# Kernel tuning notes

Measured on AMD Instinct MI355X. Metric: run time of the kernel, lower is better.

## Reference

```python
import jax, jax.numpy as jnp
import numpy as np
import math

N_HEADS = 8
D_EMBED = 512
D_CROSS = 768
D_HEAD = D_EMBED // N_HEADS


def _conv1x1(w, b, t):
    # 1x1 conv == pointwise matmul over channel dim. t: [B, Cin, H, W], w: [Cout, Cin]
    out = jnp.einsum('oc,bchw->bohw', w, t)
    return out + b[None, :, None, None]


def setup_inputs() -> dict:
    key = jax.random.key(0)
    ks = jax.random.split(key, 10)
    s = 0.02
    return {
        'x': jax.random.normal(ks[0], (8, D_EMBED, 32, 32), dtype=jnp.float32),
        'y': jax.random.normal(ks[1], (8, D_CROSS, 32, 32), dtype=jnp.float32),
        'w_q': jax.random.normal(ks[2], (D_EMBED, D_EMBED), dtype=jnp.float32) * s,
        'b_q': jnp.zeros((D_EMBED,), dtype=jnp.float32),
        'w_k': jax.random.normal(ks[3], (D_EMBED, D_CROSS), dtype=jnp.float32) * s,
        'b_k': jnp.zeros((D_EMBED,), dtype=jnp.float32),
        'w_v': jax.random.normal(ks[4], (D_EMBED, D_CROSS), dtype=jnp.float32) * s,
        'b_v': jnp.zeros((D_EMBED,), dtype=jnp.float32),
        'w_o': jax.random.normal(ks[5], (D_EMBED, D_EMBED), dtype=jnp.float32) * s,
        'b_o': jnp.zeros((D_EMBED,), dtype=jnp.float32),
    }


def reference(x, y, w_q, b_q, w_k, b_k, w_v, b_v, w_o, b_o):
    B, C, H, W = x.shape
    N = H * W
    q = _conv1x1(w_q, b_q, x)  # [B, C, H, W]
    k = _conv1x1(w_k, b_k, y)
    v = _conv1x1(w_v, b_v, y)
    # flat reshape [B, C, H, W] -> [B, nH, d_head, N] (row-major, matches torch .view)
    q = q.reshape(B, N_HEADS, D_HEAD, N)
    k = k.reshape(B, N_HEADS, D_HEAD, N)
    v = v.reshape(B, N_HEADS, D_HEAD, N)
    # attn = q^T k / sqrt(d_head): [B, nH, N, N]
    scores = jnp.einsum('bhdq,bhdk->bhqk', q, k) / math.sqrt(D_HEAD)
    attn = jax.nn.softmax(scores, axis=-1)
    # out = attn @ v^T : [B, nH, N, d_head]
    out = jnp.einsum('bhqk,bhdk->bhqd', attn, v)
    # faithful quirk: flat reshape (no transpose back) to [B, C, H, W]
    out = out.reshape(B, N_HEADS * D_HEAD, H, W)
    return _conv1x1(w_o, b_o, out)
```

## Files before the change

### kernel.cpp

```cpp
#include <hip/hip_runtime.h>
#include <cstddef>
#include <cstdint>


typedef short bs8 __attribute__((ext_vector_type(8)));
typedef short bs4 __attribute__((ext_vector_type(4)));
typedef float fx4 __attribute__((ext_vector_type(4)));

#define MFMA16(a, b, c) __builtin_amdgcn_mfma_f32_16x16x32_bf16((a), (b), (c), 0, 0, 0)

#define GLOAD_LDS16(g, l)                                                  \
  __builtin_amdgcn_global_load_lds(                                        \
      (const __attribute__((address_space(1))) void*)(g),                  \
      (__attribute__((address_space(3))) void*)(l), 16, 0, 0)

__device__ __forceinline__ short f2b(float f) {
  unsigned u = __builtin_bit_cast(unsigned, f);
  u = (u + 0x7fff + ((u >> 16) & 1)) >> 16;
  return (short)u;
}

__device__ __forceinline__ unsigned cvt_pk_bf16(float lo, float hi) {
  unsigned r;
  asm("v_cvt_pk_bf16_f32 %0, %1, %2" : "=v"(r) : "v"(lo), "v"(hi));
  return r;
}

__device__ __forceinline__ float exp2_fast(float x) {
  float r;
  asm("v_exp_f32 %0, %1" : "=v"(r) : "v"(x));
  return r;
}

#define QSCALE 0.1803368801111244f

__global__ __launch_bounds__(256) void prep(
    const float* __restrict__ w_q, const float* __restrict__ w_k,
    const float* __restrict__ w_v, const float* __restrict__ w_o,
    short* __restrict__ wdst,
    const float* __restrict__ x, short* __restrict__ xt,
    const float* __restrict__ y, short* __restrict__ yt)
{
  __shared__ short T[64][72];
  const int bid = blockIdx.x;
  const int t = threadIdx.x;

  if (bid < 1280) {
    const int i = bid * 1024 + t * 4;
    const float* src; int off;
    if (i < 262144)       { src = w_q; off = 0; }
    else if (i < 655360)  { src = w_k; off = 262144; }
    else if (i < 1048576) { src = w_v; off = 655360; }
    else                  { src = w_o; off = 1048576; }
    float4 f = *(const float4*)(src + (i - off));
    bs4 o; o[0] = f2b(f.x); o[1] = f2b(f.y); o[2] = f2b(f.z); o[3] = f2b(f.w);
    *(bs4*)(wdst + i) = o;
    return;
  }

  const float* src; short* dst; int C, nt, ct, b;
  if (bid < 2304) {
    const int local = bid - 1280;
    src = x; dst = xt; C = 512;
    nt = local & 15; ct = (local >> 4) & 7; b = local >> 7;
  } else {
    const int local = bid - 2304;
    src = y; dst = yt; C = 768;
    nt = local & 15; const int rest = local >> 4; ct = rest % 12; b = rest / 12;
  }

  const size_t srcBase = ((size_t)b * C + ct * 64) * 1024 + nt * 64;
  #pragma unroll
  for (int p = 0; p < 4; ++p) {
    const int lin = p * 256 + t;
    const int row = lin >> 4;
    const int seg = lin & 15;
    float4 f = *(const float4*)(src + srcBase + (size_t)row * 1024 + seg * 4);
    T[seg * 4 + 0][row] = f2b(f.x);
    T[seg * 4 + 1][row] = f2b(f.y);
    T[seg * 4 + 2][row] = f2b(f.z);
    T[seg * 4 + 3][row] = f2b(f.w);
  }
  __syncthreads();
  const size_t dstBase = ((size_t)b * 1024 + nt * 64) * C + ct * 64;
  #pragma unroll
  for (int p = 0; p < 2; ++p) {
    const int lin = p * 256 + t;
    const int row = lin >> 3;
    const int seg = lin & 7;
    *(bs8*)(dst + dstBase + (size_t)row * C + seg * 8) = *(const bs8*)&T[row][seg * 8];
  }
}

__global__ __launch_bounds__(256) void tcast_b(
    const short* __restrict__ src, short* __restrict__ dst, int C)
{
  __shared__ short T[64][72];
  const int t = threadIdx.x;
  const int nt = blockIdx.x, ct = blockIdx.y, b = blockIdx.z;
  const size_t srcBase = ((size_t)b * C + ct * 64) * 1024 + nt * 64;
  #pragma unroll
  for (int p = 0; p < 4; ++p) {
    const int lin = p * 256 + t;
    const int row = lin >> 4;
    const int seg = lin & 15;
    bs4 v = *(const bs4*)(src + srcBase + (size_t)row * 1024 + seg * 4);
    #pragma unroll
    for (int j = 0; j < 4; ++j) T[seg * 4 + j][row] = v[j];
  }
  __syncthreads();
  const size_t dstBase = ((size_t)b * 1024 + nt * 64) * C + ct * 64;
  #pragma unroll
  for (int p = 0; p < 2; ++p) {
    const int lin = p * 256 + t;
    const int row = lin >> 3;
    const int seg = lin & 7;
    *(bs8*)(dst + dstBase + (size_t)row * C + seg * 8) = *(const bs8*)&T[row][seg * 8];
  }
}

template<int MODE, int MTL2>
__device__ __forceinline__ void gemm2_body(
    short* As0, short* As1, short* Bs0, short* Bs1, int hw, int tid,
    const short* __restrict__ W, const short* __restrict__ Xt,
    const float* __restrict__ bias, const float* __restrict__ bias2,
    void* __restrict__ Cout, void* __restrict__ Cout2, int K, float scale)
{
  const int wid = tid >> 6, l = tid & 63;
  const int swz = (hw & 7) * (8 << MTL2) + (hw >> 3);
  const int n0 = (swz & 7) * 128;
  const int m0 = ((swz >> 3) & ((1 << MTL2) - 1)) * 128;
  const int b  = swz >> (3 + MTL2);
  const int wm = wid >> 2, wn = wid & 3;

  const int lrow = l >> 3;
  const int swz8 = ((l & 7) ^ lrow) * 8;
  const int x7 = l & 7;

  const short* Wg = W + (size_t)m0 * K;
  const short* Xg = Xt + ((size_t)b * 1024 + n0) * K;

  fx4 acc[4][2] = {};
  const int NK = K >> 6;

  #pragma unroll
  for (int j = 0; j < 2; ++j) {
    const int rb = j * 64 + wid * 8;
    const int row = rb + lrow;
    GLOAD_LDS16(Wg + (size_t)row * K + swz8, As0 + rb * 64);
    GLOAD_LDS16(Xg + (size_t)row * K + swz8, Bs0 + rb * 64);
  }
  __syncthreads();

  auto gstep = [&](const short* AsC, const short* BsC, short* AsN, short* BsN,
                   int kn, bool pre) {
    if (pre) {
      #pragma unroll
      for (int j = 0; j < 2; ++j) {
        const int rb = j * 64 + wid * 8;
        const int row = rb + lrow;
        GLOAD_LDS16(Wg + (size_t)row * K + kn + swz8, AsN + rb * 64);
        GLOAD_LDS16(Xg + (size_t)row * K + kn + swz8, BsN + rb * 64);
      }
    }
    #pragma unroll
    for (int kb = 0; kb < 2; ++kb) {
      bs8 af[4], bfr[2];
      const int u = (kb * 4 + (l >> 4)) ^ x7;
      #pragma unroll
      for (int ms = 0; ms < 4; ++ms) {
        const int rr = wm * 64 + ms * 16 + (l & 15);
        af[ms] = *(const bs8*)&AsC[rr * 64 + u * 8];
      }
      #pragma unroll
      for (int ns = 0; ns < 2; ++ns) {
        const int rr = wn * 32 + ns * 16 + (l & 15);
        bfr[ns] = *(const bs8*)&BsC[rr * 64 + u * 8];
      }
      #pragma unroll
      for (int ms = 0; ms < 4; ++ms)
        #pragma unroll
        for (int ns = 0; ns < 2; ++ns)
          acc[ms][ns] = MFMA16(af[ms], bfr[ns], acc[ms][ns]);
    }
    __syncthreads();
  };

  const int NK2 = NK >> 1;
  for (int p = 0; p < NK2; ++p) {
    gstep(As0, Bs0, As1, Bs1, (2 * p + 1) * 64, true);
    gstep(As1, Bs1, As0, Bs0, (2 * p + 2) * 64, (2 * p + 2) < NK);
  }

  #pragma unroll
  for (int ms = 0; ms < 4; ++ms) {
    #pragma unroll
    for (int ns = 0; ns < 2; ++ns) {
      const int n = n0 + wn * 32 + ns * 16 + (l & 15);
      const int mb = m0 + wm * 64 + ms * 16 + (l >> 4) * 4;
      if (MODE == 0) {
        const float f0 = (acc[ms][ns][0] + bias[mb + 0]) * scale;
        const float f1 = (acc[ms][ns][1] + bias[mb + 1]) * scale;
        const float f2 = (acc[ms][ns][2] + bias[mb + 2]) * scale;
        const float f3 = (acc[ms][ns][3] + bias[mb + 3]) * scale;
        uint2 od; od.x = cvt_pk_bf16(f0, f1); od.y = cvt_pk_bf16(f2, f3);
        short* dst = (short*)Cout + (((size_t)b * 8 + (mb >> 6)) * 1024 + n) * 64 + (mb & 63);
        *(uint2*)dst = od;
      } else if (MODE == 2) {
        #pragma unroll
        for (int r = 0; r < 4; ++r)
          ((float*)Cout)[((size_t)b * 512 + mb + r) * 1024 + n] = acc[ms][ns][r] + bias[mb + r];
      } else {
        if (mb < 512) {
          const float f0 = acc[ms][ns][0] + bias[mb + 0];
          const float f1 = acc[ms][ns][1] + bias[mb + 1];
          const float f2 = acc[ms][ns][2] + bias[mb + 2];
          const float f3 = acc[ms][ns][3] + bias[mb + 3];
          uint2 od; od.x = cvt_pk_bf16(f0, f1); od.y = cvt_pk_bf16(f2, f3);
          short* dst = (short*)Cout + (((size_t)b * 8 + (mb >> 6)) * 1024 + n) * 64 + (mb & 63);
          *(uint2*)dst = od;
        } else {
          const int c = mb - 512;
          #pragma unroll
          for (int r = 0; r < 4; ++r)
            ((short*)Cout2)[((size_t)b * 512 + c + r) * 1024 + n] = f2b(acc[ms][ns][r] + bias2[c + r]);
        }
      }
    }
  }
}

__global__ __launch_bounds__(512) void gemm_qkv(
    const short* __restrict__ wq, const short* __restrict__ wkv,
    const short* __restrict__ xt, const short* __restrict__ yt,
    const float* __restrict__ b_q, const float* __restrict__ b_k,
    const float* __restrict__ b_v,
    short* __restrict__ Qw, short* __restrict__ Kw, short* __restrict__ Vw)
{
  __shared__ short As[2][128 * 64];
  __shared__ short Bs[2][128 * 64];
  if (blockIdx.x < 256)
    gemm2_body<0, 2>(As[0], As[1], Bs[0], Bs[1], blockIdx.x, threadIdx.x,
                     wq, xt, b_q, nullptr, (void*)Qw, nullptr, 512, QSCALE);
  else
    gemm2_body<3, 3>(As[0], As[1], Bs[0], Bs[1], blockIdx.x - 256, threadIdx.x,
                     wkv, yt, b_k, b_v, (void*)Kw, (void*)Vw, 768, 1.0f);
}

__global__ __launch_bounds__(512) void gemm_o(
    const short* __restrict__ wo, const short* __restrict__ Ot,
    const float* __restrict__ b_o, float* __restrict__ out)
{
  __shared__ short As[2][128 * 64];
  __shared__ short Bs[2][128 * 64];
  gemm2_body<2, 2>(As[0], As[1], Bs[0], Bs[1], blockIdx.x, threadIdx.x,
                   wo, Ot, b_o, nullptr, (void*)out, nullptr, 512, 1.0f);
}

__global__ __launch_bounds__(256) void attn_mfma(
    const short* __restrict__ Q, const short* __restrict__ Kt,
    const short* __restrict__ V, short* __restrict__ O)
{
  __shared__ short Ks[2][64 * 64];
  __shared__ short Vs[2][64 * 64];
  __shared__ short Ps[4][16 * 64];

  const int t = threadIdx.x, wid = t >> 6, l = t & 63;
  const int hw = blockIdx.x;
  const int swzb = (hw & 7) * 128 + (hw >> 3);
  const int qt = swzb & 15, h = (swzb >> 4) & 7, b = swzb >> 7;
  const int q0 = qt * 64 + wid * 16;
  const size_t bh = (size_t)b * 8 + h;

  const short* Qg = Q + (bh * 1024 + q0) * 64;
  const short* Kg = Kt + bh * 1024 * 64;
  const short* Vg = V + bh * 64 * 1024;

  const int g = l >> 4;
  const int q = l & 15;
  const int x7 = q & 7;
  const int lrow = l >> 3;
  const int swz8 = ((l & 7) ^ lrow) * 8;
  short* Pw = Ps[wid];

  bs8 qf[2];
  #pragma unroll
  for (int db = 0; db < 2; ++db)
    qf[db] = *(const bs8*)(Qg + (size_t)q * 64 + db * 32 + g * 8);

  #pragma unroll
  for (int j = 0; j < 2; ++j) {
    const int rbase = wid * 16 + j * 8;
    const int row = rbase + lrow;
    GLOAD_LDS16(Kg + (size_t)row * 64 + swz8, &Ks[0][rbase * 64]);
    GLOAD_LDS16(Vg + (size_t)row * 1024 + swz8, &Vs[0][rbase * 64]);
  }
  __syncthreads();

  float l_part = 0.f;
  fx4 oacc[4] = {};

  auto tile = [&](const short* KsC, const short* VsC, short* KsN, short* VsN,
                  int ktn, bool pre) {
    if (pre) {
      const int k0n = ktn * 64;
      #pragma unroll
      for (int j = 0; j < 2; ++j) {
        const int rbase = wid * 16 + j * 8;
        const int row = rbase + lrow;
        GLOAD_LDS16(Kg + (size_t)(k0n + row) * 64 + swz8, KsN + rbase * 64);
        GLOAD_LDS16(Vg + (size_t)row * 1024 + k0n + swz8, VsN + rbase * 64);
      }
    }

    fx4 s[4] = {};
    __builtin_amdgcn_s_setprio(1);
    #pragma unroll
    for (int ks = 0; ks < 4; ++ks) {
      const int rr = ks * 16 + q;
      #pragma unroll
      for (int db = 0; db < 2; ++db) {
        bs8 kf = *(const bs8*)&KsC[rr * 64 + ((db * 4 + g) ^ x7) * 8];
        s[ks] = MFMA16(kf, qf[db], s[ks]);
      }
    }
    __builtin_amdgcn_s_setprio(0);

    #pragma unroll
    for (int ks = 0; ks < 4; ++ks)
      #pragma unroll
      for (int r = 0; r < 4; ++r) {
        const float e = exp2_fast(s[ks][r]);
        s[ks][r] = e;
        l_part += e;
      }

    #pragma unroll
    for (int ks = 0; ks < 4; ++ks) {
      uint2 pd;
      pd.x = cvt_pk_bf16(s[ks][0], s[ks][1]);
      pd.y = cvt_pk_bf16(s[ks][2], s[ks][3]);
      const int u16 = ks * 2 + (g >> 1);
      *(uint2*)&Pw[q * 64 + (u16 ^ x7) * 8 + (g & 1) * 4] = pd;
    }

    __builtin_amdgcn_s_setprio(1);
    #pragma unroll
    for (int kb = 0; kb < 2; ++kb) {
      const int u = kb * 4 + g;
      bs8 pf = *(const bs8*)&Pw[q * 64 + (u ^ x7) * 8];
      #pragma unroll
      for (int ds = 0; ds < 4; ++ds) {
        const int d = ds * 16 + q;
        bs8 vf = *(const bs8*)&VsC[d * 64 + (u ^ x7) * 8];
        oacc[ds] = MFMA16(pf, vf, oacc[ds]);
      }
    }
    __builtin_amdgcn_s_setprio(0);
    __syncthreads();
  };

  #pragma unroll 1
  for (int p = 0; p < 8; ++p) {
    tile(Ks[0], Vs[0], Ks[1], Vs[1], 2 * p + 1, true);
    tile(Ks[1], Vs[1], Ks[0], Vs[0], 2 * p + 2, p < 7);
  }

  l_part += __shfl_xor(l_part, 16);
  l_part += __shfl_xor(l_part, 32);
  float linv[4];
  #pragma unroll
  for (int r = 0; r < 4; ++r) linv[r] = 1.f / __shfl(l_part, g * 4 + r);
  short* Og = O + (bh * 1024 + q0) * 64;
  #pragma unroll
  for (int ds = 0; ds < 4; ++ds) {
    const int d = ds * 16 + q;
    #pragma unroll
    for (int r = 0; r < 4; ++r)
      Og[(size_t)(g * 4 + r) * 64 + d] = f2b(oacc[ds][r] * linv[r]);
  }
}

extern "C" void kernel_launch(void* const* d_in, const int* in_sizes, int n_in,
                              void* d_out, int out_size, void* d_ws, size_t ws_size,
                              hipStream_t stream) {
  const float* x   = (const float*)d_in[0];
  const float* y   = (const float*)d_in[1];
  const float* w_q = (const float*)d_in[2];
  const float* b_q = (const float*)d_in[3];
  const float* w_k = (const float*)d_in[4];
  const float* b_k = (const float*)d_in[5];
  const float* w_v = (const float*)d_in[6];
  const float* b_v = (const float*)d_in[7];
  const float* w_o = (const float*)d_in[8];
  const float* b_o = (const float*)d_in[9];

  char* ws = (char*)d_ws;
  const size_t MiB = 1u << 20;
  short* xt  = (short*)(ws);
  short* yt  = (short*)(ws + 8 * MiB);
  short* Qw  = (short*)(ws + 20 * MiB);
  short* Kw  = (short*)(ws + 28 * MiB);
  short* Vw  = (short*)(ws + 36 * MiB);
  short* Ow  = (short*)(ws + 44 * MiB);
  short* Ot  = (short*)(ws + 52 * MiB);
  short* wqb = (short*)(ws + 60 * MiB);
  short* wkb = wqb + 262144;
  short* wob = wkb + 786432;

  hipLaunchKernelGGL(prep, dim3(3840), dim3(256), 0, stream,
                     w_q, w_k, w_v, w_o, wqb, x, xt, y, yt);
  hipLaunchKernelGGL(gemm_qkv, dim3(768), dim3(512), 0, stream,
                     wqb, wkb, xt, yt, b_q, b_k, b_v, Qw, Kw, Vw);
  hipLaunchKernelGGL(attn_mfma, dim3(1024), dim3(256), 0, stream, Qw, Kw, Vw, Ow);
  hipLaunchKernelGGL(tcast_b, dim3(16, 8, 8), dim3(256), 0, stream, Ow, Ot, 512);
  hipLaunchKernelGGL(gemm_o, dim3(256), dim3(512), 0, stream, wob, Ot, b_o, (float*)d_out);
}
```

Before: 83.42 us.

## Use 8-wave attention blocks and compute row sums with a ones-vector MFMA

The attention kernel now runs 512-thread blocks covering 128 queries, so each K/V tile staged in LDS is shared by eight waves instead of four. Each wave issues half as many global-to-LDS loads per tile, and the grid halves to 512 blocks. The softmax denominator is now accumulated by an MFMA of the bf16 P fragment against a ones vector, replacing per-element float adds and cross-lane shuffles. The trade-offs are fewer blocks in flight, more waves waiting at each barrier, and a row sum built from rounded bf16 probabilities rather than fp32 values.

```diff
diff --git a/kernel.cpp b/kernel.cpp
--- a/kernel.cpp
+++ b/kernel.cpp
@@ -257,19 +257,19 @@
                    wo, Ot, b_o, nullptr, (void*)out, nullptr, 512, 1.0f);
 }
 
-__global__ __launch_bounds__(256) void attn_mfma(
+__global__ __launch_bounds__(512) void attn_mfma(
     const short* __restrict__ Q, const short* __restrict__ Kt,
     const short* __restrict__ V, short* __restrict__ O)
 {
   __shared__ short Ks[2][64 * 64];
   __shared__ short Vs[2][64 * 64];
-  __shared__ short Ps[4][16 * 64];
+  __shared__ short Ps[8][16 * 64];
 
   const int t = threadIdx.x, wid = t >> 6, l = t & 63;
   const int hw = blockIdx.x;
-  const int swzb = (hw & 7) * 128 + (hw >> 3);
-  const int qt = swzb & 15, h = (swzb >> 4) & 7, b = swzb >> 7;
-  const int q0 = qt * 64 + wid * 16;
+  const int swzb = (hw & 7) * 64 + (hw >> 3);
+  const int qt = swzb & 7, h = (swzb >> 3) & 7, b = swzb >> 6;
+  const int q0 = qt * 128 + wid * 16;
   const size_t bh = (size_t)b * 8 + h;
 
   const short* Qg = Q + (bh * 1024 + q0) * 64;
@@ -283,34 +283,30 @@
   const int swz8 = ((l & 7) ^ lrow) * 8;
   short* Pw = Ps[wid];
 
+  const bs8 onesf = {0x3F80, 0x3F80, 0x3F80, 0x3F80, 0x3F80, 0x3F80, 0x3F80, 0x3F80};
+
   bs8 qf[2];
   #pragma unroll
   for (int db = 0; db < 2; ++db)
     qf[db] = *(const bs8*)(Qg + (size_t)q * 64 + db * 32 + g * 8);
 
-  #pragma unroll
-  for (int j = 0; j < 2; ++j) {
-    const int rbase = wid * 16 + j * 8;
-    const int row = rbase + lrow;
-    GLOAD_LDS16(Kg + (size_t)row * 64 + swz8, &Ks[0][rbase * 64]);
-    GLOAD_LDS16(Vg + (size_t)row * 1024 + swz8, &Vs[0][rbase * 64]);
+  {
+    const int row = wid * 8 + lrow;
+    GLOAD_LDS16(Kg + (size_t)row * 64 + swz8, &Ks[0][wid * 8 * 64]);
+    GLOAD_LDS16(Vg + (size_t)row * 1024 + swz8, &Vs[0][wid * 8 * 64]);
   }
   __syncthreads();
 
-  float l_part = 0.f;
   fx4 oacc[4] = {};
+  fx4 lacc = {};
 
   auto tile = [&](const short* KsC, const short* VsC, short* KsN, short* VsN,
                   int ktn, bool pre) {
     if (pre) {
       const int k0n = ktn * 64;
-      #pragma unroll
-      for (int j = 0; j < 2; ++j) {
-        const int rbase = wid * 16 + j * 8;
-        const int row = rbase + lrow;
-        GLOAD_LDS16(Kg + (size_t)(k0n + row) * 64 + swz8, KsN + rbase * 64);
-        GLOAD_LDS16(Vg + (size_t)row * 1024 + k0n + swz8, VsN + rbase * 64);
-      }
+      const int row = wid * 8 + lrow;
+      GLOAD_LDS16(Kg + (size_t)(k0n + row) * 64 + swz8, KsN + wid * 8 * 64);
+      GLOAD_LDS16(Vg + (size_t)row * 1024 + k0n + swz8, VsN + wid * 8 * 64);
     }
 
     fx4 s[4] = {};
@@ -329,11 +325,8 @@
     #pragma unroll
     for (int ks = 0; ks < 4; ++ks)
       #pragma unroll
-      for (int r = 0; r < 4; ++r) {
-        const float e = exp2_fast(s[ks][r]);
-        s[ks][r] = e;
-        l_part += e;
-      }
+      for (int r = 0; r < 4; ++r)
+        s[ks][r] = exp2_fast(s[ks][r]);
 
     #pragma unroll
     for (int ks = 0; ks < 4; ++ks) {
@@ -349,6 +342,7 @@
     for (int kb = 0; kb < 2; ++kb) {
       const int u = kb * 4 + g;
       bs8 pf = *(const bs8*)&Pw[q * 64 + (u ^ x7) * 8];
+      lacc = MFMA16(pf, onesf, lacc);
       #pragma unroll
       for (int ds = 0; ds < 4; ++ds) {
         const int d = ds * 16 + q;
@@ -366,11 +360,9 @@
     tile(Ks[1], Vs[1], Ks[0], Vs[0], 2 * p + 2, p < 7);
   }
 
-  l_part += __shfl_xor(l_part, 16);
-  l_part += __shfl_xor(l_part, 32);
   float linv[4];
   #pragma unroll
-  for (int r = 0; r < 4; ++r) linv[r] = 1.f / __shfl(l_part, g * 4 + r);
+  for (int r = 0; r < 4; ++r) linv[r] = 1.f / lacc[r];
   short* Og = O + (bh * 1024 + q0) * 64;
   #pragma unroll
   for (int ds = 0; ds < 4; ++ds) {
@@ -412,7 +404,7 @@
                      w_q, w_k, w_v, w_o, wqb, x, xt, y, yt);
   hipLaunchKernelGGL(gemm_qkv, dim3(768), dim3(512), 0, stream,
                      wqb, wkb, xt, yt, b_q, b_k, b_v, Qw, Kw, Vw);
-  hipLaunchKernelGGL(attn_mfma, dim3(1024), dim3(256), 0, stream, Qw, Kw, Vw, Ow);
+  hipLaunchKernelGGL(attn_mfma, dim3(512), dim3(512), 0, stream, Qw, Kw, Vw, Ow);
   hipLaunchKernelGGL(tcast_b, dim3(16, 8, 8), dim3(256), 0, stream, Ow, Ot, 512);
   hipLaunchKernelGGL(gemm_o, dim3(256), dim3(512), 0, stream, wob, Ot, b_o, (float*)d_out);
 }
```

Result: faster. 79.56 us (-4.6%).
